# Kernel tuning notes

Hardware: AMD Instinct MI355X
Metric: run time of the kernel (lower is better)

Reference implementation:

```python
import jax, jax.numpy as jnp
import numpy as np

KSIZE = 7
PAD = KSIZE // 2          # reflection pad radius
EPS_BN = 1e-5             # CONFIG.model.arch.batchnorm_eps
SCALE = 1.0               # self.scale
BN_W, BN_B = 0.1, 0.0     # BatchNorm init per module


def _l2n(x, eps=1e-12):
    return x / (jnp.linalg.norm(x) + eps)


def setup_inputs() -> dict:
    key = jax.random.key(0)
    ks = jax.random.split(key, 6)
    B, Cg, Co, H, W = 2, 128, 32, 512, 512
    f = jax.random.normal(ks[0], (B, Cg, H, W), jnp.float32)
    alpha = jax.random.normal(ks[1], (B, Co, H, W), jnp.float32)
    # guidance_conv: 1x1 conv Cg -> Cg//2 (xavier-ish init)
    wg = jax.random.normal(ks[2], (Cg // 2, Cg), jnp.float32) * (1.0 / np.sqrt(Cg))
    bg = jnp.zeros((Cg // 2,), jnp.float32)
    # spectral-norm 1x1 conv Co -> Co, no bias
    w_bar = jax.random.normal(ks[3], (Co, Co), jnp.float32) * (1.0 / np.sqrt(Co))
    u = _l2n(jax.random.normal(ks[4], (Co,), jnp.float32))
    v = _l2n(jax.random.normal(ks[5], (Co,), jnp.float32))
    return {"f": f, "alpha": alpha, "wg": wg, "bg": bg, "w_bar": w_bar, "u": u, "v": v}


def reference(f, alpha, wg, bg, w_bar, u, v):
    B, _, H, W = f.shape
    # 1x1 guidance conv
    g = jnp.einsum('oc,bchw->bohw', wg, f) + bg[None, :, None, None]
    # hop_normalize: channel-wise L2 normalize, clamped at 1e-4
    gn = g / jnp.maximum(jnp.linalg.norm(g, axis=1, keepdims=True), 1e-4)
    r = jnp.pad(gn, ((0, 0), (0, 0), (PAD, PAD), (PAD, PAD)), mode='reflect')
    # ksize^2 shifted-window correlation -> scores [K2, B, 1, H, W]
    scores = []
    for i in range(KSIZE):
        for j in range(KSIZE):
            if i == PAD and j == PAD:
                scores.append(jnp.full((B, 1, H, W), -10000.0, gn.dtype))
            else:
                scores.append((gn * r[:, :, i:i + H, j:j + W]).sum(axis=1, keepdims=True))
    s = jax.nn.softmax(jnp.stack(scores, axis=0) * SCALE, axis=0)
    # weighted neighborhood aggregation of alpha (skip center tap)
    alp = jnp.pad(alpha, ((0, 0), (0, 0), (PAD, PAD), (PAD, PAD)), mode='reflect')
    y = jnp.zeros_like(alpha)
    for i in range(KSIZE):
        for j in range(KSIZE):
            if i == PAD and j == PAD:
                continue
            y = y + alp[:, :, i:i + H, j:j + W] * s[i * KSIZE + j]
    # spectral-norm 1x1 conv (training: one detached power iteration)
    v1 = jax.lax.stop_gradient(_l2n(w_bar.T @ u))
    u1 = jax.lax.stop_gradient(_l2n(w_bar @ v1))
    sigma = u1 @ (w_bar @ v1)
    w_sn = w_bar / sigma
    y2 = jnp.einsum('oc,bchw->bohw', w_sn, y)
    # BatchNorm2d, training mode (batch stats), weight=0.1 bias=0
    mean = y2.mean(axis=(0, 2, 3), keepdims=True)
    var = y2.var(axis=(0, 2, 3), keepdims=True)
    y_bn = BN_W * (y2 - mean) / jnp.sqrt(var + EPS_BN) + BN_B
    return y_bn + alpha
```

## Files before the change

kernel.cpp:

```cpp
#include <hip/hip_runtime.h>

#define HWc   262144
#define CGc   128
#define CHc   64
#define COc   32
#define NPIXc 524288
#define TW 32
#define TH 8
#define HLW 38
#define HLH 14
#define HPX (HLW*HLH)

typedef _Float16 h2 __attribute__((ext_vector_type(2)));

__device__ __forceinline__ int refl(int p){
  if (p < 0) p = -p;
  else if (p >= 512) p = 1022 - p;
  return p;
}
__device__ __forceinline__ h2 as_h2(unsigned u){ union{unsigned u; h2 h;} x; x.u = u; return x.h; }
__device__ __forceinline__ unsigned as_u(h2 h){ union{unsigned u; h2 h;} x; x.h = h; return x.u; }
__device__ __forceinline__ unsigned pkh(float a, float b){
  h2 h; h.x = (_Float16)a; h.y = (_Float16)b; return as_u(h);
}
__device__ __forceinline__ float2 upk(unsigned u){
  h2 h = as_h2(u); return make_float2((float)h.x, (float)h.y);
}
__device__ __forceinline__ float dot2h(unsigned a, unsigned b, float c){
  return __builtin_amdgcn_fdot2(as_h2(a), as_h2(b), c, false);
}
__device__ __forceinline__ float2 pkfma(float2 a, float2 b, float2 c){
  float2 d;
  asm("v_pk_fma_f32 %0, %1, %2, %3" : "=v"(d) : "v"(a), "v"(b), "v"(c));
  return d;
}

__global__ void k0_prep(const float* __restrict__ wbar, const float* __restrict__ u,
                        const float* __restrict__ wg,
                        unsigned* __restrict__ wsnb, unsigned* __restrict__ wgb){
  const int t = threadIdx.x;
  __shared__ float sv1[32];
  float tv = 0.f;
  if (t < 32){
    #pragma unroll
    for (int o = 0; o < 32; o++) tv += wbar[o*32 + t] * u[o];
  }
  float sq = tv * tv;
  #pragma unroll
  for (int off = 32; off; off >>= 1) sq += __shfl_down(sq, off);
  const float n1 = sqrtf(__shfl(sq, 0)) + 1e-12f;
  if (t < 32) sv1[t] = tv / n1;
  __syncthreads();
  float tu = 0.f;
  if (t < 32){
    #pragma unroll
    for (int c = 0; c < 32; c++) tu += wbar[t*32 + c] * sv1[c];
  }
  float sq2 = tu * tu;
  #pragma unroll
  for (int off = 32; off; off >>= 1) sq2 += __shfl_down(sq2, off);
  const float S = __shfl(sq2, 0);
  const float inv = (sqrtf(S) + 1e-12f) / S;
  for (int k = t; k < 512; k += 64){
    const int o = k >> 4, p = k & 15;
    wsnb[k] = pkh(wbar[o*32 + 2*p] * inv, wbar[o*32 + 2*p + 1] * inv);
  }
  for (int k = t; k < 4096; k += 64){
    const int o = k >> 6, p = k & 63;
    wgb[k] = pkh(wg[o*128 + 2*p], wg[o*128 + 2*p + 1]);
  }
}

__global__ __launch_bounds__(256) void k1_gn(const float* __restrict__ f,
                                             const unsigned* __restrict__ wgb,
                                             const float* __restrict__ bg,
                                             unsigned* __restrict__ gn){
  const int p   = blockIdx.x * 256 + threadIdx.x;
  const int b   = p >> 18;
  const int pix = p & (HWc - 1);
  const float* fb = f + (size_t)b * CGc * HWc + pix;

  float acc[CHc];
  #pragma unroll
  for (int o = 0; o < CHc; o++) acc[o] = bg[o];

  #pragma unroll 1
  for (int pp = 0; pp < 64; pp += 4){
    unsigned fp[4];
    #pragma unroll
    for (int m = 0; m < 4; m++)
      fp[m] = pkh(fb[(size_t)(2*(pp+m)) * HWc], fb[(size_t)(2*(pp+m)+1) * HWc]);
    #pragma unroll
    for (int o = 0; o < CHc; o++){
      float a = acc[o];
      a = dot2h(fp[0], wgb[o*64 + pp + 0], a);
      a = dot2h(fp[1], wgb[o*64 + pp + 1], a);
      a = dot2h(fp[2], wgb[o*64 + pp + 2], a);
      a = dot2h(fp[3], wgb[o*64 + pp + 3], a);
      acc[o] = a;
    }
  }
  float nsq = 0.f;
  #pragma unroll
  for (int o = 0; o < CHc; o++) nsq = fmaf(acc[o], acc[o], nsq);
  const float inv = 1.f / fmaxf(sqrtf(nsq), 1e-4f);

  uint4* gp = (uint4*)(gn + (size_t)p * 32);
  #pragma unroll
  for (int k = 0; k < 8; k++){
    uint4 w;
    w.x = pkh(acc[8*k+0]*inv, acc[8*k+1]*inv);
    w.y = pkh(acc[8*k+2]*inv, acc[8*k+3]*inv);
    w.z = pkh(acc[8*k+4]*inv, acc[8*k+5]*inv);
    w.w = pkh(acc[8*k+6]*inv, acc[8*k+7]*inv);
    gp[k] = w;
  }
}

__global__ __launch_bounds__(256) void k2a_at(const float* __restrict__ alpha,
                                              const unsigned* __restrict__ wsnb,
                                              unsigned* __restrict__ apm){
  const int p   = blockIdx.x * 256 + threadIdx.x;
  const int b   = p >> 18;
  const int pix = p & (HWc - 1);
  const float* ab = alpha + (size_t)b * COc * HWc + pix;
  unsigned a16[16];
  #pragma unroll
  for (int k = 0; k < 16; k++)
    a16[k] = pkh(ab[(size_t)(2*k) * HWc], ab[(size_t)(2*k+1) * HWc]);
  unsigned ow[16];
  #pragma unroll
  for (int o = 0; o < COc; o += 2){
    float s0 = 0.f, s1 = 0.f;
    #pragma unroll
    for (int k = 0; k < 16; k++){
      s0 = dot2h(a16[k], wsnb[(o+0)*16 + k], s0);
      s1 = dot2h(a16[k], wsnb[(o+1)*16 + k], s1);
    }
    ow[o >> 1] = pkh(s0, s1);
  }
  uint4* op = (uint4*)(apm + (size_t)p * 16);
  #pragma unroll
  for (int k = 0; k < 4; k++)
    op[k] = make_uint4(ow[4*k], ow[4*k+1], ow[4*k+2], ow[4*k+3]);
}

__global__ __launch_bounds__(256) void k2_agg(const unsigned* __restrict__ gn,
                                              const unsigned* __restrict__ apm,
                                              unsigned* __restrict__ y2){
  __shared__ uint4 gs4[8][HPX];

  const int lb  = (blockIdx.x & 7) * 256 + (blockIdx.x >> 3);
  const int txx = lb & 15;
  const int tyy = (lb >> 4) & 63;
  const int bb  = lb >> 10;
  const int x0  = txx * TW, y0 = tyy * TH;
  const int tid = threadIdx.x;

  for (int t = tid; t < HPX; t += 256){
    const int hr = t / HLW;
    const int hc = t - hr * HLW;
    const int gy = refl(y0 + hr - 3);
    const int gx = refl(x0 + hc - 3);
    const uint4* src = (const uint4*)(gn + (size_t)((bb << 18) + (gy << 9) + gx) * 32);
    #pragma unroll
    for (int k = 0; k < 8; k++) gs4[k][t] = src[k];
  }
  __syncthreads();

  const int r  = tid >> 5, c = tid & 31;
  const int yy = y0 + r,  xx = x0 + c;
  const int self = (r + 3) * HLW + (c + 3);

  uint4 cv[8];
  #pragma unroll
  for (int k = 0; k < 8; k++) cv[k] = gs4[k][self];

  int ax[7];
  #pragma unroll
  for (int j = 0; j < 7; j++) ax[j] = refl(xx + j - 3);

  float2 yac[16];
  #pragma unroll
  for (int k = 0; k < 16; k++) yac[k] = make_float2(0.f, 0.f);
  float esum = 0.f;

  #pragma unroll 1
  for (int i = 0; i < 7; i++){
    const int ay = refl(yy + i - 3);
    const unsigned* aprow = apm + (size_t)((bb << 18) + (ay << 9)) * 16;
    const int rowbase = (r + i) * HLW + c;
    #pragma unroll
    for (int j = 0; j < 7; j++){
      if (i == 3 && j == 3) continue;
      const int hp = rowbase + j;
      float s0 = 0.f, s1 = 0.f, s2 = 0.f, s3 = 0.f;
      #pragma unroll
      for (int k = 0; k < 8; k++){
        const uint4 q = gs4[k][hp];
        s0 = dot2h(cv[k].x, q.x, s0);
        s1 = dot2h(cv[k].y, q.y, s1);
        s2 = dot2h(cv[k].z, q.z, s2);
        s3 = dot2h(cv[k].w, q.w, s3);
      }
      const float e = __expf((s0 + s1) + (s2 + s3));
      esum += e;
      const float2 e2 = make_float2(e, e);
      const uint4* ap = (const uint4*)(aprow + (size_t)ax[j] * 16);
      #pragma unroll
      for (int kk = 0; kk < 4; kk++){
        const uint4 a = ap[kk];
        yac[4*kk+0] = pkfma(upk(a.x), e2, yac[4*kk+0]);
        yac[4*kk+1] = pkfma(upk(a.y), e2, yac[4*kk+1]);
        yac[4*kk+2] = pkfma(upk(a.z), e2, yac[4*kk+2]);
        yac[4*kk+3] = pkfma(upk(a.w), e2, yac[4*kk+3]);
      }
    }
  }

  const float inv = 1.f / esum;
  unsigned yw[16];
  #pragma unroll
  for (int k = 0; k < 16; k++) yw[k] = pkh(yac[k].x * inv, yac[k].y * inv);
  uint4* yp = (uint4*)(y2 + (size_t)((bb << 18) + (yy << 9) + xx) * 16);
  #pragma unroll
  for (int k = 0; k < 4; k++)
    yp[k] = make_uint4(yw[4*k], yw[4*k+1], yw[4*k+2], yw[4*k+3]);
}

__global__ __launch_bounds__(256) void k3_stats(const unsigned* __restrict__ y2,
                                                float* __restrict__ stats){
  float s[COc], q[COc];
  #pragma unroll
  for (int o = 0; o < COc; o++){ s[o] = 0.f; q[o] = 0.f; }
  const int stride = gridDim.x * 256;
  for (int p = blockIdx.x * 256 + threadIdx.x; p < NPIXc; p += stride){
    const uint4* yp = (const uint4*)(y2 + (size_t)p * 16);
    #pragma unroll
    for (int k = 0; k < 4; k++){
      const uint4 w = yp[k];
      const unsigned vv[4] = {w.x, w.y, w.z, w.w};
      #pragma unroll
      for (int m = 0; m < 4; m++){
        const float2 ab = upk(vv[m]);
        s[8*k+2*m]   += ab.x; q[8*k+2*m]   = fmaf(ab.x, ab.x, q[8*k+2*m]);
        s[8*k+2*m+1] += ab.y; q[8*k+2*m+1] = fmaf(ab.y, ab.y, q[8*k+2*m+1]);
      }
    }
  }
  #pragma unroll
  for (int o = 0; o < COc; o++){
    #pragma unroll
    for (int off = 32; off; off >>= 1){
      s[o] += __shfl_down(s[o], off);
      q[o] += __shfl_down(q[o], off);
    }
  }
  __shared__ float red[4][64];
  const int wv = threadIdx.x >> 6;
  if ((threadIdx.x & 63) == 0){
    #pragma unroll
    for (int o = 0; o < COc; o++){ red[wv][o] = s[o]; red[wv][32 + o] = q[o]; }
  }
  __syncthreads();
  if (threadIdx.x < 64){
    const float v = red[0][threadIdx.x] + red[1][threadIdx.x]
                  + red[2][threadIdx.x] + red[3][threadIdx.x];
    atomicAdd(&stats[threadIdx.x], v);
  }
}

__global__ void k3b_final(const float* __restrict__ stats, float* __restrict__ stats2){
  const int t = threadIdx.x;
  if (t < COc){
    const float invN = 1.f / (float)NPIXc;
    const float mean = stats[t] * invN;
    const float var  = fmaf(-mean, mean, stats[COc + t] * invN);
    stats2[t]       = mean;
    stats2[COc + t] = 0.1f * rsqrtf(var + 1e-5f);
  }
}

__global__ __launch_bounds__(256) void k4_out(const unsigned* __restrict__ y2,
                                              const float* __restrict__ alpha,
                                              const float* __restrict__ stats2,
                                              float* __restrict__ out){
  const int p   = blockIdx.x * 256 + threadIdx.x;
  const int b   = p >> 18;
  const int pix = p & (HWc - 1);
  const uint4* yp = (const uint4*)(y2 + (size_t)p * 16);
  const size_t boff = (size_t)b * COc * HWc + pix;
  #pragma unroll
  for (int k = 0; k < 4; k++){
    const uint4 w = yp[k];
    const unsigned vv[4] = {w.x, w.y, w.z, w.w};
    #pragma unroll
    for (int m = 0; m < 4; m++){
      const int o = 8*k + 2*m;
      const float2 ab = upk(vv[m]);
      out[boff + (size_t)o*HWc]     = fmaf(ab.x - stats2[o],   stats2[COc+o],
                                           alpha[boff + (size_t)o*HWc]);
      out[boff + (size_t)(o+1)*HWc] = fmaf(ab.y - stats2[o+1], stats2[COc+o+1],
                                           alpha[boff + (size_t)(o+1)*HWc]);
    }
  }
}

extern "C" void kernel_launch(void* const* d_in, const int* in_sizes, int n_in,
                              void* d_out, int out_size, void* d_ws, size_t ws_size,
                              hipStream_t stream){
  const float* f     = (const float*)d_in[0];
  const float* alpha = (const float*)d_in[1];
  const float* wg    = (const float*)d_in[2];
  const float* bg    = (const float*)d_in[3];
  const float* wbar  = (const float*)d_in[4];
  const float* u     = (const float*)d_in[5];
  (void)in_sizes; (void)n_in; (void)out_size; (void)ws_size;
  float* out = (float*)d_out;

  char* ws = (char*)d_ws;
  float*    stats  = (float*)ws;
  float*    stats2 = (float*)(ws + 4096);
  unsigned* wsnb   = (unsigned*)(ws + 8192);
  unsigned* wgb    = (unsigned*)(ws + 16384);
  unsigned* apm    = (unsigned*)(ws + 65536);
  unsigned* gn     = (unsigned*)(ws + 65536 + (size_t)NPIXc*64);
  unsigned* y2     = (unsigned*)(ws + 65536 + (size_t)NPIXc*64 + (size_t)NPIXc*128);

  hipMemsetAsync(stats, 0, 64 * sizeof(float), stream);
  k0_prep  <<<1, 64, 0, stream>>>(wbar, u, wg, wsnb, wgb);
  k1_gn    <<<NPIXc / 256, 256, 0, stream>>>(f, wgb, bg, gn);
  k2a_at   <<<NPIXc / 256, 256, 0, stream>>>(alpha, wsnb, apm);
  k2_agg   <<<2048, 256, 0, stream>>>(gn, apm, y2);
  k3_stats <<<256, 256, 0, stream>>>(y2, stats);
  k3b_final<<<1, 64, 0, stream>>>(stats, stats2);
  k4_out   <<<NPIXc / 256, 256, 0, stream>>>(y2, alpha, stats2, out);
}
```

Measured before the change: 330.0 us.

## Fuse guidance and alpha projection kernels, fold BN stats into aggregation, use fma_mix

Merges the guidance-conv/normalize kernel with the alpha spectral-norm projection into one launch. BatchNorm sum and sum-of-squares are now computed inside the aggregation kernel from in-register results, which removes the separate stats pass that re-read y2. The packed f32 FMA on unpacked halves is replaced with v_fma_mix_f32, which consumes fp16 lanes directly and so drops the conversion instructions. The trade-off is higher register pressure in both fused kernels, 32 extra shuffle reductions per block, and one atomic per block in the aggregation kernel.

```diff
diff --git a/kernel.cpp b/kernel.cpp
--- a/kernel.cpp
+++ b/kernel.cpp
@@ -29,10 +29,13 @@
 __device__ __forceinline__ float dot2h(unsigned a, unsigned b, float c){
   return __builtin_amdgcn_fdot2(as_h2(a), as_h2(b), c, false);
 }
-__device__ __forceinline__ float2 pkfma(float2 a, float2 b, float2 c){
-  float2 d;
-  asm("v_pk_fma_f32 %0, %1, %2, %3" : "=v"(d) : "v"(a), "v"(b), "v"(c));
-  return d;
+__device__ __forceinline__ void mixlo(float& acc, unsigned ab, float e){
+  asm("v_fma_mix_f32 %0, %1, %2, %0 op_sel:[0,0,0] op_sel_hi:[1,0,0]"
+      : "+v"(acc) : "v"(ab), "v"(e));
+}
+__device__ __forceinline__ void mixhi(float& acc, unsigned ab, float e){
+  asm("v_fma_mix_f32 %0, %1, %2, %0 op_sel:[1,0,0] op_sel_hi:[1,0,0]"
+      : "+v"(acc) : "v"(ab), "v"(e));
 }
 
 __global__ void k0_prep(const float* __restrict__ wbar, const float* __restrict__ u,
@@ -71,10 +74,13 @@
   }
 }
 
-__global__ __launch_bounds__(256) void k1_gn(const float* __restrict__ f,
-                                             const unsigned* __restrict__ wgb,
-                                             const float* __restrict__ bg,
-                                             unsigned* __restrict__ gn){
+__global__ __launch_bounds__(256) void k1f(const float* __restrict__ f,
+                                           const float* __restrict__ alpha,
+                                           const unsigned* __restrict__ wgb,
+                                           const unsigned* __restrict__ wsnb,
+                                           const float* __restrict__ bg,
+                                           unsigned* __restrict__ gn,
+                                           unsigned* __restrict__ apm){
   const int p   = blockIdx.x * 256 + threadIdx.x;
   const int b   = p >> 18;
   const int pix = p & (HWc - 1);
@@ -115,14 +121,7 @@
     w.w = pkh(acc[8*k+6]*inv, acc[8*k+7]*inv);
     gp[k] = w;
   }
-}
-
-__global__ __launch_bounds__(256) void k2a_at(const float* __restrict__ alpha,
-                                              const unsigned* __restrict__ wsnb,
-                                              unsigned* __restrict__ apm){
-  const int p   = blockIdx.x * 256 + threadIdx.x;
-  const int b   = p >> 18;
-  const int pix = p & (HWc - 1);
+
   const float* ab = alpha + (size_t)b * COc * HWc + pix;
   unsigned a16[16];
   #pragma unroll
@@ -147,8 +146,10 @@
 
 __global__ __launch_bounds__(256) void k2_agg(const unsigned* __restrict__ gn,
                                               const unsigned* __restrict__ apm,
-                                              unsigned* __restrict__ y2){
+                                              unsigned* __restrict__ y2,
+                                              float* __restrict__ stats){
   __shared__ uint4 gs4[8][HPX];
+  __shared__ float red[4][64];
 
   const int lb  = (blockIdx.x & 7) * 256 + (blockIdx.x >> 3);
   const int txx = lb & 15;
@@ -180,9 +181,9 @@
   #pragma unroll
   for (int j = 0; j < 7; j++) ax[j] = refl(xx + j - 3);
 
-  float2 yac[16];
-  #pragma unroll
-  for (int k = 0; k < 16; k++) yac[k] = make_float2(0.f, 0.f);
+  float yac[COc];
+  #pragma unroll
+  for (int k = 0; k < COc; k++) yac[k] = 0.f;
   float esum = 0.f;
 
   #pragma unroll 1
@@ -205,68 +206,51 @@
       }
       const float e = __expf((s0 + s1) + (s2 + s3));
       esum += e;
-      const float2 e2 = make_float2(e, e);
       const uint4* ap = (const uint4*)(aprow + (size_t)ax[j] * 16);
       #pragma unroll
       for (int kk = 0; kk < 4; kk++){
         const uint4 a = ap[kk];
-        yac[4*kk+0] = pkfma(upk(a.x), e2, yac[4*kk+0]);
-        yac[4*kk+1] = pkfma(upk(a.y), e2, yac[4*kk+1]);
-        yac[4*kk+2] = pkfma(upk(a.z), e2, yac[4*kk+2]);
-        yac[4*kk+3] = pkfma(upk(a.w), e2, yac[4*kk+3]);
+        mixlo(yac[8*kk+0], a.x, e); mixhi(yac[8*kk+1], a.x, e);
+        mixlo(yac[8*kk+2], a.y, e); mixhi(yac[8*kk+3], a.y, e);
+        mixlo(yac[8*kk+4], a.z, e); mixhi(yac[8*kk+5], a.z, e);
+        mixlo(yac[8*kk+6], a.w, e); mixhi(yac[8*kk+7], a.w, e);
       }
     }
   }
 
   const float inv = 1.f / esum;
+  float yn[COc];
   unsigned yw[16];
   #pragma unroll
-  for (int k = 0; k < 16; k++) yw[k] = pkh(yac[k].x * inv, yac[k].y * inv);
+  for (int k = 0; k < 16; k++){
+    yn[2*k]   = yac[2*k]   * inv;
+    yn[2*k+1] = yac[2*k+1] * inv;
+    yw[k] = pkh(yn[2*k], yn[2*k+1]);
+  }
   uint4* yp = (uint4*)(y2 + (size_t)((bb << 18) + (yy << 9) + xx) * 16);
   #pragma unroll
   for (int k = 0; k < 4; k++)
     yp[k] = make_uint4(yw[4*k], yw[4*k+1], yw[4*k+2], yw[4*k+3]);
-}
-
-__global__ __launch_bounds__(256) void k3_stats(const unsigned* __restrict__ y2,
-                                                float* __restrict__ stats){
-  float s[COc], q[COc];
-  #pragma unroll
-  for (int o = 0; o < COc; o++){ s[o] = 0.f; q[o] = 0.f; }
-  const int stride = gridDim.x * 256;
-  for (int p = blockIdx.x * 256 + threadIdx.x; p < NPIXc; p += stride){
-    const uint4* yp = (const uint4*)(y2 + (size_t)p * 16);
-    #pragma unroll
-    for (int k = 0; k < 4; k++){
-      const uint4 w = yp[k];
-      const unsigned vv[4] = {w.x, w.y, w.z, w.w};
-      #pragma unroll
-      for (int m = 0; m < 4; m++){
-        const float2 ab = upk(vv[m]);
-        s[8*k+2*m]   += ab.x; q[8*k+2*m]   = fmaf(ab.x, ab.x, q[8*k+2*m]);
-        s[8*k+2*m+1] += ab.y; q[8*k+2*m+1] = fmaf(ab.y, ab.y, q[8*k+2*m+1]);
-      }
-    }
-  }
+
+  float sch[COc], qch[COc];
+  #pragma unroll
+  for (int o = 0; o < COc; o++){ sch[o] = yn[o]; qch[o] = yn[o] * yn[o]; }
   #pragma unroll
   for (int o = 0; o < COc; o++){
     #pragma unroll
     for (int off = 32; off; off >>= 1){
-      s[o] += __shfl_down(s[o], off);
-      q[o] += __shfl_down(q[o], off);
-    }
-  }
-  __shared__ float red[4][64];
-  const int wv = threadIdx.x >> 6;
-  if ((threadIdx.x & 63) == 0){
-    #pragma unroll
-    for (int o = 0; o < COc; o++){ red[wv][o] = s[o]; red[wv][32 + o] = q[o]; }
+      sch[o] += __shfl_down(sch[o], off);
+      qch[o] += __shfl_down(qch[o], off);
+    }
+  }
+  const int wv = tid >> 6;
+  if ((tid & 63) == 0){
+    #pragma unroll
+    for (int o = 0; o < COc; o++){ red[wv][o] = sch[o]; red[wv][32 + o] = qch[o]; }
   }
   __syncthreads();
-  if (threadIdx.x < 64){
-    const float v = red[0][threadIdx.x] + red[1][threadIdx.x]
-                  + red[2][threadIdx.x] + red[3][threadIdx.x];
-    atomicAdd(&stats[threadIdx.x], v);
+  if (tid < 64){
+    atomicAdd(&stats[tid], red[0][tid] + red[1][tid] + red[2][tid] + red[3][tid]);
   }
 }
 
@@ -329,10 +313,8 @@
 
   hipMemsetAsync(stats, 0, 64 * sizeof(float), stream);
   k0_prep  <<<1, 64, 0, stream>>>(wbar, u, wg, wsnb, wgb);
-  k1_gn    <<<NPIXc / 256, 256, 0, stream>>>(f, wgb, bg, gn);
-  k2a_at   <<<NPIXc / 256, 256, 0, stream>>>(alpha, wsnb, apm);
-  k2_agg   <<<2048, 256, 0, stream>>>(gn, apm, y2);
-  k3_stats <<<256, 256, 0, stream>>>(y2, stats);
+  k1f      <<<NPIXc / 256, 256, 0, stream>>>(f, alpha, wgb, wsnb, bg, gn, apm);
+  k2_agg   <<<2048, 256, 0, stream>>>(gn, apm, y2, stats);
   k3b_final<<<1, 64, 0, stream>>>(stats, stats2);
   k4_out   <<<NPIXc / 256, 256, 0, stream>>>(y2, alpha, stats2, out);
 }
```

Result: slower. 338.7 us (+2.6%).

## Fuse guidance and alpha-transform kernels, split aggregation LDS tile into two channel halves

Applied to the files above, without the earlier changes.

Merges the guidance-conv/normalize kernel with the alpha spectral-norm transform kernel, so one launch and one pass over pixel indices does both. In the aggregation kernel the shared-memory halo of normalized guidance is loaded in two 32-channel halves, which halves LDS use to allow more resident blocks; partial scores from the first half are kept in 48 registers. The accumulation now uses v_fma_mix_f32 straight from packed fp16 instead of unpacking and v_pk_fma, and the tap loop is fully unrolled. The trade-off is more register pressure from the saved scores, a second barrier, and a second read of the halo from global memory.

```diff
diff --git a/kernel.cpp b/kernel.cpp
--- a/kernel.cpp
+++ b/kernel.cpp
@@ -29,10 +29,13 @@
 __device__ __forceinline__ float dot2h(unsigned a, unsigned b, float c){
   return __builtin_amdgcn_fdot2(as_h2(a), as_h2(b), c, false);
 }
-__device__ __forceinline__ float2 pkfma(float2 a, float2 b, float2 c){
-  float2 d;
-  asm("v_pk_fma_f32 %0, %1, %2, %3" : "=v"(d) : "v"(a), "v"(b), "v"(c));
-  return d;
+__device__ __forceinline__ void mixlo(float& acc, unsigned ab, float e){
+  asm("v_fma_mix_f32 %0, %1, %2, %0 op_sel:[0,0,0] op_sel_hi:[1,0,0]"
+      : "+v"(acc) : "v"(ab), "v"(e));
+}
+__device__ __forceinline__ void mixhi(float& acc, unsigned ab, float e){
+  asm("v_fma_mix_f32 %0, %1, %2, %0 op_sel:[1,0,0] op_sel_hi:[1,0,0]"
+      : "+v"(acc) : "v"(ab), "v"(e));
 }
 
 __global__ void k0_prep(const float* __restrict__ wbar, const float* __restrict__ u,
@@ -71,10 +74,13 @@
   }
 }
 
-__global__ __launch_bounds__(256) void k1_gn(const float* __restrict__ f,
-                                             const unsigned* __restrict__ wgb,
-                                             const float* __restrict__ bg,
-                                             unsigned* __restrict__ gn){
+__global__ __launch_bounds__(256) void k1f(const float* __restrict__ f,
+                                           const float* __restrict__ alpha,
+                                           const unsigned* __restrict__ wgb,
+                                           const unsigned* __restrict__ wsnb,
+                                           const float* __restrict__ bg,
+                                           unsigned* __restrict__ gn,
+                                           unsigned* __restrict__ apm){
   const int p   = blockIdx.x * 256 + threadIdx.x;
   const int b   = p >> 18;
   const int pix = p & (HWc - 1);
@@ -115,14 +121,7 @@
     w.w = pkh(acc[8*k+6]*inv, acc[8*k+7]*inv);
     gp[k] = w;
   }
-}
-
-__global__ __launch_bounds__(256) void k2a_at(const float* __restrict__ alpha,
-                                              const unsigned* __restrict__ wsnb,
-                                              unsigned* __restrict__ apm){
-  const int p   = blockIdx.x * 256 + threadIdx.x;
-  const int b   = p >> 18;
-  const int pix = p & (HWc - 1);
+
   const float* ab = alpha + (size_t)b * COc * HWc + pix;
   unsigned a16[16];
   #pragma unroll
@@ -148,7 +147,7 @@
 __global__ __launch_bounds__(256) void k2_agg(const unsigned* __restrict__ gn,
                                               const unsigned* __restrict__ apm,
                                               unsigned* __restrict__ y2){
-  __shared__ uint4 gs4[8][HPX];
+  __shared__ uint4 gs4[4][HPX];
 
   const int lb  = (blockIdx.x & 7) * 256 + (blockIdx.x >> 3);
   const int txx = lb & 15;
@@ -157,6 +156,10 @@
   const int x0  = txx * TW, y0 = tyy * TH;
   const int tid = threadIdx.x;
 
+  const int r  = tid >> 5, c = tid & 31;
+  const int yy = y0 + r,  xx = x0 + c;
+  const int self = (r + 3) * HLW + (c + 3);
+
   for (int t = tid; t < HPX; t += 256){
     const int hr = t / HLW;
     const int hc = t - hr * HLW;
@@ -164,39 +167,69 @@
     const int gx = refl(x0 + hc - 3);
     const uint4* src = (const uint4*)(gn + (size_t)((bb << 18) + (gy << 9) + gx) * 32);
     #pragma unroll
-    for (int k = 0; k < 8; k++) gs4[k][t] = src[k];
-  }
-  __syncthreads();
-
-  const int r  = tid >> 5, c = tid & 31;
-  const int yy = y0 + r,  xx = x0 + c;
-  const int self = (r + 3) * HLW + (c + 3);
-
-  uint4 cv[8];
-  #pragma unroll
-  for (int k = 0; k < 8; k++) cv[k] = gs4[k][self];
+    for (int k = 0; k < 4; k++) gs4[k][t] = src[k];
+  }
+  __syncthreads();
+
+  uint4 cv[4];
+  #pragma unroll
+  for (int k = 0; k < 4; k++) cv[k] = gs4[k][self];
+
+  float sc[49];
+  #pragma unroll
+  for (int i = 0; i < 7; i++){
+    #pragma unroll
+    for (int j = 0; j < 7; j++){
+      if (i == 3 && j == 3) continue;
+      const int hp = (r + i) * HLW + (c + j);
+      float s0 = 0.f, s1 = 0.f, s2 = 0.f, s3 = 0.f;
+      #pragma unroll
+      for (int k = 0; k < 4; k++){
+        const uint4 q = gs4[k][hp];
+        s0 = dot2h(cv[k].x, q.x, s0);
+        s1 = dot2h(cv[k].y, q.y, s1);
+        s2 = dot2h(cv[k].z, q.z, s2);
+        s3 = dot2h(cv[k].w, q.w, s3);
+      }
+      sc[i*7+j] = (s0 + s1) + (s2 + s3);
+    }
+  }
+  __syncthreads();
+
+  for (int t = tid; t < HPX; t += 256){
+    const int hr = t / HLW;
+    const int hc = t - hr * HLW;
+    const int gy = refl(y0 + hr - 3);
+    const int gx = refl(x0 + hc - 3);
+    const uint4* src = (const uint4*)(gn + (size_t)((bb << 18) + (gy << 9) + gx) * 32);
+    #pragma unroll
+    for (int k = 0; k < 4; k++) gs4[k][t] = src[k + 4];
+  }
+  __syncthreads();
+
+  #pragma unroll
+  for (int k = 0; k < 4; k++) cv[k] = gs4[k][self];
 
   int ax[7];
   #pragma unroll
   for (int j = 0; j < 7; j++) ax[j] = refl(xx + j - 3);
 
-  float2 yac[16];
-  #pragma unroll
-  for (int k = 0; k < 16; k++) yac[k] = make_float2(0.f, 0.f);
+  float yac[COc];
+  #pragma unroll
+  for (int k = 0; k < COc; k++) yac[k] = 0.f;
   float esum = 0.f;
 
-  #pragma unroll 1
+  #pragma unroll
   for (int i = 0; i < 7; i++){
     const int ay = refl(yy + i - 3);
     const unsigned* aprow = apm + (size_t)((bb << 18) + (ay << 9)) * 16;
-    const int rowbase = (r + i) * HLW + c;
     #pragma unroll
     for (int j = 0; j < 7; j++){
       if (i == 3 && j == 3) continue;
-      const int hp = rowbase + j;
-      float s0 = 0.f, s1 = 0.f, s2 = 0.f, s3 = 0.f;
+      const int hp = (r + i) * HLW + (c + j);
+      float s0 = sc[i*7+j], s1 = 0.f, s2 = 0.f, s3 = 0.f;
       #pragma unroll
-      for (int k = 0; k < 8; k++){
+      for (int k = 0; k < 4; k++){
         const uint4 q = gs4[k][hp];
         s0 = dot2h(cv[k].x, q.x, s0);
         s1 = dot2h(cv[k].y, q.y, s1);
@@ -205,15 +238,14 @@
       }
       const float e = __expf((s0 + s1) + (s2 + s3));
       esum += e;
-      const float2 e2 = make_float2(e, e);
       const uint4* ap = (const uint4*)(aprow + (size_t)ax[j] * 16);
       #pragma unroll
       for (int kk = 0; kk < 4; kk++){
         const uint4 a = ap[kk];
-        yac[4*kk+0] = pkfma(upk(a.x), e2, yac[4*kk+0]);
-        yac[4*kk+1] = pkfma(upk(a.y), e2, yac[4*kk+1]);
-        yac[4*kk+2] = pkfma(upk(a.z), e2, yac[4*kk+2]);
-        yac[4*kk+3] = pkfma(upk(a.w), e2, yac[4*kk+3]);
+        mixlo(yac[8*kk+0], a.x, e); mixhi(yac[8*kk+1], a.x, e);
+        mixlo(yac[8*kk+2], a.y, e); mixhi(yac[8*kk+3], a.y, e);
+        mixlo(yac[8*kk+4], a.z, e); mixhi(yac[8*kk+5], a.z, e);
+        mixlo(yac[8*kk+6], a.w, e); mixhi(yac[8*kk+7], a.w, e);
       }
     }
   }
@@ -221,7 +253,7 @@
   const float inv = 1.f / esum;
   unsigned yw[16];
   #pragma unroll
-  for (int k = 0; k < 16; k++) yw[k] = pkh(yac[k].x * inv, yac[k].y * inv);
+  for (int k = 0; k < 16; k++) yw[k] = pkh(yac[2*k] * inv, yac[2*k+1] * inv);
   uint4* yp = (uint4*)(y2 + (size_t)((bb << 18) + (yy << 9) + xx) * 16);
   #pragma unroll
   for (int k = 0; k < 4; k++)
@@ -329,8 +361,7 @@
 
   hipMemsetAsync(stats, 0, 64 * sizeof(float), stream);
   k0_prep  <<<1, 64, 0, stream>>>(wbar, u, wg, wsnb, wgb);
-  k1_gn    <<<NPIXc / 256, 256, 0, stream>>>(f, wgb, bg, gn);
-  k2a_at   <<<NPIXc / 256, 256, 0, stream>>>(alpha, wsnb, apm);
+  k1f      <<<NPIXc / 256, 256, 0, stream>>>(f, alpha, wgb, wsnb, bg, gn, apm);
   k2_agg   <<<2048, 256, 0, stream>>>(gn, apm, y2);
   k3_stats <<<256, 256, 0, stream>>>(y2, stats);
   k3b_final<<<1, 64, 0, stream>>>(stats, stats2);
```

Result: slower. 590.1 us (+78.8%).
